# Kernel optimization log

Measured on AMD Instinct MI355X. Metric: run time of the kernel, lower is better.

Reference implementation:

```python
import jax, jax.numpy as jnp
import numpy as np

D_MODEL = 1024
N_HEADS = 16
HEAD_DIM = D_MODEL // N_HEADS
D_FF = 4096
EPS = 1e-5


def _layer_norm(x, gamma, beta):
    mu = jnp.mean(x, axis=-1, keepdims=True)
    var = jnp.var(x, axis=-1, keepdims=True)
    return (x - mu) * jax.lax.rsqrt(var + EPS) * gamma + beta


def setup_inputs() -> dict:
    key = jax.random.key(0)
    ks = jax.random.split(key, 16)
    B, T, S = 2, 2048, 2048
    s = 1.0 / np.sqrt(D_MODEL)
    inp = {
        "tgt": jax.random.normal(ks[0], (B, T, D_MODEL), jnp.float32),
        "memory": jax.random.normal(ks[1], (B, S, D_MODEL), jnp.float32),
        "wq": jax.random.normal(ks[2], (D_MODEL, D_MODEL), jnp.float32) * s,
        "bq": jnp.zeros((D_MODEL,), jnp.float32),
        "wk": jax.random.normal(ks[3], (D_MODEL, D_MODEL), jnp.float32) * s,
        "bk": jnp.zeros((D_MODEL,), jnp.float32),
        "wv": jax.random.normal(ks[4], (D_MODEL, D_MODEL), jnp.float32) * s,
        "bv": jnp.zeros((D_MODEL,), jnp.float32),
        "wo": jax.random.normal(ks[5], (D_MODEL, D_MODEL), jnp.float32) * s,
        "bo": jnp.zeros((D_MODEL,), jnp.float32),
        "w1": jax.random.normal(ks[6], (D_MODEL, D_FF), jnp.float32) * s,
        "b1": jnp.zeros((D_FF,), jnp.float32),
        "w2": jax.random.normal(ks[7], (D_FF, D_MODEL), jnp.float32) * (1.0 / np.sqrt(D_FF)),
        "b2": jnp.zeros((D_MODEL,), jnp.float32),
        "g1": jnp.ones((D_MODEL,), jnp.float32),
        "be1": jnp.zeros((D_MODEL,), jnp.float32),
        "g2": jnp.ones((D_MODEL,), jnp.float32),
        "be2": jnp.zeros((D_MODEL,), jnp.float32),
    }
    return inp


def reference(tgt, memory, wq, bq, wk, bk, wv, bv, wo, bo, w1, b1, w2, b2, g1, be1, g2, be2):
    B, T, _ = tgt.shape
    S = memory.shape[1]
    scale = HEAD_DIM ** -0.5
    # projections -> [B, H, L, Dh]
    Q = (tgt @ wq + bq).reshape(B, T, N_HEADS, HEAD_DIM).transpose(0, 2, 1, 3)
    K = (memory @ wk + bk).reshape(B, S, N_HEADS, HEAD_DIM).transpose(0, 2, 1, 3)
    V = (memory @ wv + bv).reshape(B, S, N_HEADS, HEAD_DIM).transpose(0, 2, 1, 3)
    scores = jnp.einsum("bhtd,bhsd->bhts", Q, K) * scale
    attn = jax.nn.softmax(scores, axis=-1)  # dropout=0 (eval)
    ctx = jnp.einsum("bhts,bhsd->bhtd", attn, V)
    ctx = ctx.transpose(0, 2, 1, 3).reshape(B, T, D_MODEL)
    attn_out = ctx @ wo + bo
    # post-norm residual blocks
    x = _layer_norm(tgt + attn_out, g1, be1)
    ff = jax.nn.relu(x @ w1 + b1) @ w2 + b2
    out = _layer_norm(x + ff, g2, be2)
    return out
```

## Files before the change

kernel.cpp:

```cpp
#include <hip/hip_runtime.h>


typedef unsigned short u16;
typedef __attribute__((ext_vector_type(8))) short bvec8;
typedef __attribute__((ext_vector_type(4))) float fvec4;

#define MFMA16(a, b, c) __builtin_amdgcn_mfma_f32_16x16x32_bf16((a), (b), (c), 0, 0, 0)

__device__ __forceinline__ u16 f2b(float f) {
  union { float f; unsigned u; } x; x.f = f;
  unsigned u = x.u;
  return (u16)((u + 0x7FFFu + ((u >> 16) & 1u)) >> 16);
}
__device__ __forceinline__ u16 f2b_t(float f) {
  union { float f; unsigned u; } x; x.f = f;
  return (u16)(x.u >> 16);
}
__device__ __forceinline__ void gl_lds16(const u16* g, u16* lds) {
  __builtin_amdgcn_global_load_lds(
      (const __attribute__((address_space(1))) void*)g,
      (__attribute__((address_space(3))) void*)lds, 16, 0, 0);
}

__global__ __launch_bounds__(256) void k_tobf(const float* __restrict__ in,
                                              u16* __restrict__ out, int n4) {
  int i = blockIdx.x * 256 + threadIdx.x;
  if (i >= n4) return;
  float4 v = ((const float4*)in)[i];
  ushort4 o;
  o.x = f2b(v.x); o.y = f2b(v.y); o.z = f2b(v.z); o.w = f2b(v.w);
  ((ushort4*)out)[i] = o;
}

__global__ __launch_bounds__(256) void k_wt(const float* __restrict__ W,
                                            u16* __restrict__ WT, int K, int N) {
  __shared__ float t[32][33];
  int tx = threadIdx.x & 31, ty = threadIdx.x >> 5;
  int n0 = blockIdx.x * 32, k0 = blockIdx.y * 32;
#pragma unroll
  for (int i = 0; i < 4; i++)
    t[ty + i * 8][tx] = W[(size_t)(k0 + ty + i * 8) * N + n0 + tx];
  __syncthreads();
#pragma unroll
  for (int i = 0; i < 4; i++)
    WT[(size_t)(n0 + ty + i * 8) * K + k0 + tx] = f2b(t[tx][ty + i * 8]);
}

__global__ __launch_bounds__(256) void k_vt(const u16* __restrict__ V,
                                            u16* __restrict__ Vt) {
  __shared__ u16 t[32][33];
  int tx = threadIdx.x & 31, ty = threadIdx.x >> 5;
  int s0 = blockIdx.x * 32, d0 = blockIdx.y * 32, bh = blockIdx.z;
  int b = bh >> 4, h = bh & 15;
#pragma unroll
  for (int i = 0; i < 4; i++)
    t[ty + i * 8][tx] = V[(size_t)(b * 2048 + s0 + ty + i * 8) * 1024 + h * 64 + d0 + tx];
  __syncthreads();
#pragma unroll
  for (int i = 0; i < 4; i++)
    Vt[((size_t)bh * 64 + d0 + ty + i * 8) * 2048 + s0 + tx] = t[tx][ty + i * 8];
}

template <int TM, int TN>
__global__ __launch_bounds__(256, 3) void k_gemm(
    const u16* __restrict__ A, const u16* __restrict__ BT,
    const float* __restrict__ bias, const float* __restrict__ bias2,
    const float* __restrict__ resid, float* __restrict__ outF,
    u16* __restrict__ outB, u16* __restrict__ outB2,
    int M, int N, int K, float scale, int flags) {
  constexpr int WM = TM / 2, WN = TN / 2;
  constexpr int MI = WM / 16, NI = WN / 16;
  constexpr int NCALL = (TM + TN) / 64;
  __shared__ u16 S[(TM + TN) * 32];
  const int tid = threadIdx.x, w = tid >> 6, lane = tid & 63;
  const int q = lane >> 4, l = lane & 15;
  const int m0 = blockIdx.y * TM, n0 = blockIdx.x * TN;
  const int wm = (w >> 1) * WM, wn = (w & 1) * WN;
  const int srow = lane >> 2, sgrp = lane & 3;
  const int gcol = ((sgrp + (srow >> 1)) & 3) * 8;
  const int rpos = ((q + 4 - ((l >> 1) & 3)) & 3) * 8;
  const u16* gp[NCALL];
  u16* lp[NCALL];
#pragma unroll
  for (int c = 0; c < NCALL; c++) {
    int r0 = (w * NCALL + c) * 16;
    gp[c] = (r0 < TM) ? A + (size_t)(m0 + r0 + srow) * K + gcol
                      : BT + (size_t)(n0 + r0 - TM + srow) * K + gcol;
    lp[c] = &S[r0 * 32];
  }
  fvec4 acc[MI][NI] = {};
#pragma unroll 1
  for (int k0 = 0; k0 < K; k0 += 32) {
#pragma unroll
    for (int c = 0; c < NCALL; c++) gl_lds16(gp[c] + k0, lp[c]);
    __syncthreads();
    bvec8 af[MI], bf[NI];
#pragma unroll
    for (int i = 0; i < MI; i++)
      af[i] = *(const bvec8*)&S[(wm + 16 * i + l) * 32 + rpos];
#pragma unroll
    for (int j = 0; j < NI; j++)
      bf[j] = *(const bvec8*)&S[(TM + wn + 16 * j + l) * 32 + rpos];
#pragma unroll
    for (int i = 0; i < MI; i++)
#pragma unroll
      for (int j = 0; j < NI; j++)
        acc[i][j] = MFMA16(af[i], bf[j], acc[i][j]);
    __syncthreads();
  }
  const int On = outB2 ? 1024 : N;
#pragma unroll
  for (int mi = 0; mi < MI; mi++)
#pragma unroll
    for (int ni = 0; ni < NI; ni++) {
      int row = m0 + wm + mi * 16 + q * 4;
      int col = n0 + wn + ni * 16 + l;
      const float* bs = bias;
      u16* ob = outB;
      float sc = scale;
      int oc = col;
      if (outB2 && col >= 1024) { bs = bias2; ob = outB2; sc = 1.0f; oc = col - 1024; }
      float bv = bs[oc];
#pragma unroll
      for (int r = 0; r < 4; r++) {
        float v = (acc[mi][ni][r] + bv) * sc;
        if (flags & 1) v = fmaxf(v, 0.0f);
        size_t idx = (size_t)(row + r) * On + oc;
        if (flags & 8) v += resid[idx];
        if (flags & 2) ob[idx] = f2b(v);
        if (flags & 4) outF[idx] = v;
      }
    }
}

__global__ __launch_bounds__(256, 2) void k_attn(
    const u16* __restrict__ Q, const u16* __restrict__ Kb,
    const u16* __restrict__ Vt, u16* __restrict__ ctx) {
  __shared__ u16 Ks[64 * 64];
  __shared__ u16 Vs[64 * 64];
  __shared__ u16 Ps[4][2][16 * 72];
  const int tid = threadIdx.x, w = tid >> 6, lane = tid & 63;
  const int q = lane >> 4, l = lane & 15;
  const int blk = blockIdx.x;
  const int bh = blk >> 4, tb = blk & 15;
  const int b = bh >> 4, h = bh & 15;
  const int t0 = tb * 128 + w * 32;
  const u16* Qp = Q + (size_t)(b * 2048 + t0) * 1024 + h * 64;
  const u16* Kp = Kb + (size_t)(b * 2048) * 1024 + h * 64;
  const u16* Vp = Vt + (size_t)bh * 64 * 2048;
  const int rowin = lane >> 3, grp = lane & 7;
  const int gcol = ((grp + rowin) & 7) * 8;
  const int kc0 = ((q + 8 - (l & 7)) & 7) * 8;
  const int kc1 = ((q + 12 - (l & 7)) & 7) * 8;
  bvec8 aQ[2][2];
#pragma unroll
  for (int ti = 0; ti < 2; ti++)
#pragma unroll
    for (int kh = 0; kh < 2; kh++)
      aQ[ti][kh] = *(const bvec8*)&Qp[(size_t)(ti * 16 + l) * 1024 + kh * 32 + q * 8];
  fvec4 o[2][4] = {};
  float ls[2][4] = {};
#pragma unroll 1
  for (int s0 = 0; s0 < 2048; s0 += 64) {
    gl_lds16(Kp + (size_t)(s0 + w * 8 + rowin) * 1024 + gcol, &Ks[(w * 8) * 64]);
    gl_lds16(Kp + (size_t)(s0 + 32 + w * 8 + rowin) * 1024 + gcol, &Ks[(32 + w * 8) * 64]);
    gl_lds16(Vp + (size_t)(w * 8 + rowin) * 2048 + s0 + gcol, &Vs[(w * 8) * 64]);
    gl_lds16(Vp + (size_t)(32 + w * 8 + rowin) * 2048 + s0 + gcol, &Vs[(32 + w * 8) * 64]);
    __syncthreads();
    fvec4 sc[2][4];
#pragma unroll
    for (int ti = 0; ti < 2; ti++)
#pragma unroll
      for (int ss = 0; ss < 4; ss++) sc[ti][ss] = (fvec4){0.f, 0.f, 0.f, 0.f};
#pragma unroll
    for (int ss = 0; ss < 4; ss++) {
      const int ro = (ss * 16 + l) * 64;
      bvec8 kf0 = *(const bvec8*)&Ks[ro + kc0];
      bvec8 kf1 = *(const bvec8*)&Ks[ro + kc1];
#pragma unroll
      for (int ti = 0; ti < 2; ti++) {
        sc[ti][ss] = MFMA16(aQ[ti][0], kf0, sc[ti][ss]);
        sc[ti][ss] = MFMA16(aQ[ti][1], kf1, sc[ti][ss]);
      }
    }
#pragma unroll
    for (int ti = 0; ti < 2; ti++)
#pragma unroll
      for (int ss = 0; ss < 4; ss++)
#pragma unroll
        for (int r = 0; r < 4; r++) {
          float p = __expf(sc[ti][ss][r]);
          ls[ti][r] += p;
          Ps[w][ti][(q * 4 + r) * 72 + ss * 16 + l] = f2b_t(p);
        }
    asm volatile("s_waitcnt lgkmcnt(0)" ::: "memory");
    bvec8 bV[4][2];
#pragma unroll
    for (int dt = 0; dt < 4; dt++) {
      const int ro = (dt * 16 + l) * 64;
      bV[dt][0] = *(const bvec8*)&Vs[ro + kc0];
      bV[dt][1] = *(const bvec8*)&Vs[ro + kc1];
    }
#pragma unroll
    for (int ti = 0; ti < 2; ti++) {
      bvec8 aP0 = *(const bvec8*)&Ps[w][ti][l * 72 + q * 8];
      bvec8 aP1 = *(const bvec8*)&Ps[w][ti][l * 72 + 32 + q * 8];
#pragma unroll
      for (int dt = 0; dt < 4; dt++) {
        o[ti][dt] = MFMA16(aP0, bV[dt][0], o[ti][dt]);
        o[ti][dt] = MFMA16(aP1, bV[dt][1], o[ti][dt]);
      }
    }
    __syncthreads();
  }
#pragma unroll
  for (int ti = 0; ti < 2; ti++)
#pragma unroll
    for (int r = 0; r < 4; r++) {
      float s = ls[ti][r];
      s += __shfl_xor(s, 1, 64);
      s += __shfl_xor(s, 2, 64);
      s += __shfl_xor(s, 4, 64);
      s += __shfl_xor(s, 8, 64);
      float inv = 1.0f / s;
      size_t trow = (size_t)(b * 2048 + t0 + ti * 16 + q * 4 + r);
#pragma unroll
      for (int dt = 0; dt < 4; dt++)
        ctx[trow * 1024 + h * 64 + dt * 16 + l] = f2b(o[ti][dt][r] * inv);
    }
}

__global__ __launch_bounds__(256) void k_ln(
    const float* __restrict__ y, const float* __restrict__ g,
    const float* __restrict__ be, float* __restrict__ xf, u16* __restrict__ xb) {
  __shared__ float sm[8];
  int row = blockIdx.x, tid = threadIdx.x;
  const float* yr = y + (size_t)row * 1024;
  float v[4], s = 0.f, ss = 0.f;
#pragma unroll
  for (int j = 0; j < 4; j++) {
    v[j] = yr[tid + j * 256];
    s += v[j]; ss += v[j] * v[j];
  }
#pragma unroll
  for (int off = 32; off; off >>= 1) {
    s += __shfl_down(s, off, 64);
    ss += __shfl_down(ss, off, 64);
  }
  int w = tid >> 6;
  if ((tid & 63) == 0) { sm[w] = s; sm[4 + w] = ss; }
  __syncthreads();
  float S = sm[0] + sm[1] + sm[2] + sm[3];
  float SS = sm[4] + sm[5] + sm[6] + sm[7];
  float mean = S * (1.0f / 1024.0f);
  float var = SS * (1.0f / 1024.0f) - mean * mean;
  float rstd = rsqrtf(var + 1e-5f);
#pragma unroll
  for (int j = 0; j < 4; j++) {
    int c = tid + j * 256;
    float o = (v[j] - mean) * rstd * g[c] + be[c];
    xf[(size_t)row * 1024 + c] = o;
    if (xb) xb[(size_t)row * 1024 + c] = f2b(o);
  }
}

extern "C" void kernel_launch(void* const* d_in, const int* in_sizes, int n_in,
                              void* d_out, int out_size, void* d_ws, size_t ws_size,
                              hipStream_t stream) {
  (void)in_sizes; (void)n_in; (void)out_size; (void)ws_size;
  const float* tgt = (const float*)d_in[0];
  const float* mem = (const float*)d_in[1];
  const float* wq  = (const float*)d_in[2];
  const float* bq  = (const float*)d_in[3];
  const float* wk  = (const float*)d_in[4];
  const float* bk  = (const float*)d_in[5];
  const float* wv  = (const float*)d_in[6];
  const float* bv  = (const float*)d_in[7];
  const float* wo  = (const float*)d_in[8];
  const float* bo  = (const float*)d_in[9];
  const float* w1  = (const float*)d_in[10];
  const float* b1  = (const float*)d_in[11];
  const float* w2  = (const float*)d_in[12];
  const float* b2  = (const float*)d_in[13];
  const float* g1  = (const float*)d_in[14];
  const float* be1 = (const float*)d_in[15];
  const float* g2  = (const float*)d_in[16];
  const float* be2 = (const float*)d_in[17];
  float* out = (float*)d_out;

  char* ws = (char*)d_ws;
  size_t off = 0;
  auto take = [&](size_t bytes) { char* p = ws + off; off += bytes; return p; };
  const size_t MB = 1024 * 1024;
  u16* tgt_b = (u16*)take(8 * MB);
  u16* mem_b = (u16*)take(8 * MB);
  u16* wqT   = (u16*)take(2 * MB);
  u16* wkvT  = (u16*)take(4 * MB);
  u16* woT   = (u16*)take(2 * MB);
  u16* w1T   = (u16*)take(8 * MB);
  u16* w2T   = (u16*)take(8 * MB);
  u16* Qb    = (u16*)take(8 * MB);
  u16* Kb    = (u16*)take(8 * MB);
  u16* Vb    = (u16*)take(8 * MB);
  u16* Vtb   = (u16*)take(8 * MB);
  u16* ctx   = (u16*)take(8 * MB);
  float* y1  = (float*)take(16 * MB);
  float* xf  = (float*)take(16 * MB);
  u16* xb    = (u16*)take(8 * MB);
  u16* hbuf  = Qb;
  float* y2  = (float*)ctx;

  k_tobf<<<4096, 256, 0, stream>>>(tgt, tgt_b, 4096 * 1024 / 4);
  k_tobf<<<4096, 256, 0, stream>>>(mem, mem_b, 4096 * 1024 / 4);
  k_wt<<<dim3(32, 32), 256, 0, stream>>>(wq, wqT, 1024, 1024);
  k_wt<<<dim3(32, 32), 256, 0, stream>>>(wk, wkvT, 1024, 1024);
  k_wt<<<dim3(32, 32), 256, 0, stream>>>(wv, wkvT + 1024 * 1024, 1024, 1024);
  k_wt<<<dim3(32, 32), 256, 0, stream>>>(wo, woT, 1024, 1024);
  k_wt<<<dim3(128, 32), 256, 0, stream>>>(w1, w1T, 1024, 4096);
  k_wt<<<dim3(32, 128), 256, 0, stream>>>(w2, w2T, 4096, 1024);
  k_gemm<64, 128><<<dim3(8, 64), 256, 0, stream>>>(
      tgt_b, wqT, bq, nullptr, nullptr, nullptr, Qb, nullptr,
      4096, 1024, 1024, 0.125f, 2);
  k_gemm<128, 128><<<dim3(16, 32), 256, 0, stream>>>(
      mem_b, wkvT, bk, bv, nullptr, nullptr, Kb, Vb,
      4096, 2048, 1024, 1.0f, 2);
  k_vt<<<dim3(64, 2, 32), 256, 0, stream>>>(Vb, Vtb);
  k_attn<<<512, 256, 0, stream>>>(Qb, Kb, Vtb, ctx);
  k_gemm<64, 128><<<dim3(8, 64), 256, 0, stream>>>(
      ctx, woT, bo, nullptr, tgt, y1, nullptr, nullptr,
      4096, 1024, 1024, 1.0f, 4 | 8);
  k_ln<<<4096, 256, 0, stream>>>(y1, g1, be1, xf, xb);
  k_gemm<128, 128><<<dim3(32, 32), 256, 0, stream>>>(
      xb, w1T, b1, nullptr, nullptr, nullptr, hbuf, nullptr,
      4096, 4096, 1024, 1.0f, 1 | 2);
  k_gemm<64, 128><<<dim3(8, 64), 256, 0, stream>>>(
      hbuf, w2T, b2, nullptr, xf, y2, nullptr, nullptr,
      4096, 1024, 4096, 1.0f, 4 | 8);
  k_ln<<<4096, 256, 0, stream>>>(y2, g2, be2, out, nullptr);
}
```

Measured before the change: 437.6 us.

## Split-K the N=1024 GEMMs and split-KV the attention to fill more CUs

Attention now runs over two halves of the key sequence in separate blocks. Each half writes unnormalized fp32 partial outputs and row sums, and a new combine kernel adds them and normalizes to bf16. The output-projection and FFN-down GEMMs use a two-way split-K that writes fp32 partials, and a fused kernel adds the partials, bias and residual before the layernorm. Occupancy hints are also raised for the 64-row GEMM and for attention. The aim is to double the grid of launches that were under-filling the GPU, at the cost of extra fp32 partial-buffer traffic and one more launch. Skipping the softmax max is safe only if the scores stay bounded, as the original code already assumed.

```diff
diff --git a/kernel.cpp b/kernel.cpp
--- a/kernel.cpp
+++ b/kernel.cpp
@@ -62,12 +62,12 @@
 }
 
 template <int TM, int TN>
-__global__ __launch_bounds__(256, 3) void k_gemm(
+__global__ __launch_bounds__(256, TM == 64 ? 4 : 3) void k_gemm(
     const u16* __restrict__ A, const u16* __restrict__ BT,
     const float* __restrict__ bias, const float* __restrict__ bias2,
     const float* __restrict__ resid, float* __restrict__ outF,
     u16* __restrict__ outB, u16* __restrict__ outB2,
-    int M, int N, int K, float scale, int flags) {
+    int M, int N, int Kstride, int Klen, float scale, int flags) {
   constexpr int WM = TM / 2, WN = TN / 2;
   constexpr int MI = WM / 16, NI = WN / 16;
   constexpr int NCALL = (TM + TN) / 64;
@@ -75,6 +75,7 @@
   const int tid = threadIdx.x, w = tid >> 6, lane = tid & 63;
   const int q = lane >> 4, l = lane & 15;
   const int m0 = blockIdx.y * TM, n0 = blockIdx.x * TN;
+  const int kbeg = blockIdx.z * Klen;
   const int wm = (w >> 1) * WM, wn = (w & 1) * WN;
   const int srow = lane >> 2, sgrp = lane & 3;
   const int gcol = ((sgrp + (srow >> 1)) & 3) * 8;
@@ -84,13 +85,13 @@
 #pragma unroll
   for (int c = 0; c < NCALL; c++) {
     int r0 = (w * NCALL + c) * 16;
-    gp[c] = (r0 < TM) ? A + (size_t)(m0 + r0 + srow) * K + gcol
-                      : BT + (size_t)(n0 + r0 - TM + srow) * K + gcol;
+    gp[c] = (r0 < TM) ? A + (size_t)(m0 + r0 + srow) * Kstride + kbeg + gcol
+                      : BT + (size_t)(n0 + r0 - TM + srow) * Kstride + kbeg + gcol;
     lp[c] = &S[r0 * 32];
   }
   fvec4 acc[MI][NI] = {};
 #pragma unroll 1
-  for (int k0 = 0; k0 < K; k0 += 32) {
+  for (int k0 = 0; k0 < Klen; k0 += 32) {
 #pragma unroll
     for (int c = 0; c < NCALL; c++) gl_lds16(gp[c] + k0, lp[c]);
     __syncthreads();
@@ -107,6 +108,20 @@
       for (int j = 0; j < NI; j++)
         acc[i][j] = MFMA16(af[i], bf[j], acc[i][j]);
     __syncthreads();
+  }
+  if (flags & 16) {
+    float* po = outF + (size_t)blockIdx.z * M * N;
+#pragma unroll
+    for (int mi = 0; mi < MI; mi++)
+#pragma unroll
+      for (int ni = 0; ni < NI; ni++) {
+        int row = m0 + wm + mi * 16 + q * 4;
+        int col = n0 + wn + ni * 16 + l;
+#pragma unroll
+        for (int r = 0; r < 4; r++)
+          po[(size_t)(row + r) * N + col] = acc[mi][ni][r];
+      }
+    return;
   }
   const int On = outB2 ? 1024 : N;
 #pragma unroll
@@ -133,9 +148,10 @@
     }
 }
 
-__global__ __launch_bounds__(256, 2) void k_attn(
+__global__ __launch_bounds__(256, 4) void k_attn(
     const u16* __restrict__ Q, const u16* __restrict__ Kb,
-    const u16* __restrict__ Vt, u16* __restrict__ ctx) {
+    const u16* __restrict__ Vt, float* __restrict__ opart,
+    float* __restrict__ lpart) {
   __shared__ u16 Ks[64 * 64];
   __shared__ u16 Vs[64 * 64];
   __shared__ u16 Ps[4][2][16 * 72];
@@ -145,6 +161,9 @@
   const int bh = blk >> 4, tb = blk & 15;
   const int b = bh >> 4, h = bh & 15;
   const int t0 = tb * 128 + w * 32;
+  const int sbeg = blockIdx.y * 1024;
+  float* op = opart + (size_t)blockIdx.y * 4096 * 1024;
+  float* lp = lpart + (size_t)blockIdx.y * 4096 * 16;
   const u16* Qp = Q + (size_t)(b * 2048 + t0) * 1024 + h * 64;
   const u16* Kp = Kb + (size_t)(b * 2048) * 1024 + h * 64;
   const u16* Vp = Vt + (size_t)bh * 64 * 2048;
@@ -161,7 +180,7 @@
   fvec4 o[2][4] = {};
   float ls[2][4] = {};
 #pragma unroll 1
-  for (int s0 = 0; s0 < 2048; s0 += 64) {
+  for (int s0 = sbeg; s0 < sbeg + 1024; s0 += 64) {
     gl_lds16(Kp + (size_t)(s0 + w * 8 + rowin) * 1024 + gcol, &Ks[(w * 8) * 64]);
     gl_lds16(Kp + (size_t)(s0 + 32 + w * 8 + rowin) * 1024 + gcol, &Ks[(32 + w * 8) * 64]);
     gl_lds16(Vp + (size_t)(w * 8 + rowin) * 2048 + s0 + gcol, &Vs[(w * 8) * 64]);
@@ -222,24 +241,44 @@
       s += __shfl_xor(s, 2, 64);
       s += __shfl_xor(s, 4, 64);
       s += __shfl_xor(s, 8, 64);
-      float inv = 1.0f / s;
-      size_t trow = (size_t)(b * 2048 + t0 + ti * 16 + q * 4 + r);
+      int trow = b * 2048 + t0 + ti * 16 + q * 4 + r;
+      if (l == 0) lp[trow * 16 + h] = s;
 #pragma unroll
       for (int dt = 0; dt < 4; dt++)
-        ctx[trow * 1024 + h * 64 + dt * 16 + l] = f2b(o[ti][dt][r] * inv);
-    }
-}
-
-__global__ __launch_bounds__(256) void k_ln(
-    const float* __restrict__ y, const float* __restrict__ g,
-    const float* __restrict__ be, float* __restrict__ xf, u16* __restrict__ xb) {
+        op[(size_t)trow * 1024 + h * 64 + dt * 16 + l] = o[ti][dt][r];
+    }
+}
+
+__global__ __launch_bounds__(256) void k_actx(const float* __restrict__ opart,
+                                              const float* __restrict__ lpart,
+                                              u16* __restrict__ ctx) {
+  int row = blockIdx.x, c0 = threadIdx.x * 4;
+  int h = c0 >> 6;
+  float lsum = lpart[row * 16 + h] + lpart[4096 * 16 + row * 16 + h];
+  float inv = 1.0f / lsum;
+  float4 a = *(const float4*)&opart[(size_t)row * 1024 + c0];
+  float4 b = *(const float4*)&opart[(size_t)4096 * 1024 + (size_t)row * 1024 + c0];
+  ushort4 o;
+  o.x = f2b((a.x + b.x) * inv);
+  o.y = f2b((a.y + b.y) * inv);
+  o.z = f2b((a.z + b.z) * inv);
+  o.w = f2b((a.w + b.w) * inv);
+  *(ushort4*)&ctx[(size_t)row * 1024 + c0] = o;
+}
+
+__global__ __launch_bounds__(256) void k_lnp(
+    const float* __restrict__ p0, const float* __restrict__ p1,
+    const float* __restrict__ bias, const float* __restrict__ resid,
+    const float* __restrict__ g, const float* __restrict__ be,
+    float* __restrict__ xf, u16* __restrict__ xb) {
   __shared__ float sm[8];
   int row = blockIdx.x, tid = threadIdx.x;
-  const float* yr = y + (size_t)row * 1024;
+  size_t base = (size_t)row * 1024;
   float v[4], s = 0.f, ss = 0.f;
 #pragma unroll
   for (int j = 0; j < 4; j++) {
-    v[j] = yr[tid + j * 256];
+    int c = tid + j * 256;
+    v[j] = p0[base + c] + p1[base + c] + bias[c] + resid[base + c];
     s += v[j]; ss += v[j] * v[j];
   }
 #pragma unroll
@@ -259,8 +298,8 @@
   for (int j = 0; j < 4; j++) {
     int c = tid + j * 256;
     float o = (v[j] - mean) * rstd * g[c] + be[c];
-    xf[(size_t)row * 1024 + c] = o;
-    if (xb) xb[(size_t)row * 1024 + c] = f2b(o);
+    xf[base + c] = o;
+    if (xb) xb[base + c] = f2b(o);
   }
 }
 
@@ -304,11 +343,13 @@
   u16* Vb    = (u16*)take(8 * MB);
   u16* Vtb   = (u16*)take(8 * MB);
   u16* ctx   = (u16*)take(8 * MB);
-  float* y1  = (float*)take(16 * MB);
+  float* opart = (float*)take(32 * MB);
+  float* lpart = (float*)take(1 * MB);
+  float* opj   = (float*)take(32 * MB);
   float* xf  = (float*)take(16 * MB);
   u16* xb    = (u16*)take(8 * MB);
   u16* hbuf  = Qb;
-  float* y2  = (float*)ctx;
+  float* fp2 = opart;
 
   k_tobf<<<4096, 256, 0, stream>>>(tgt, tgt_b, 4096 * 1024 / 4);
   k_tobf<<<4096, 256, 0, stream>>>(mem, mem_b, 4096 * 1024 / 4);
@@ -320,21 +361,22 @@
   k_wt<<<dim3(32, 128), 256, 0, stream>>>(w2, w2T, 4096, 1024);
   k_gemm<64, 128><<<dim3(8, 64), 256, 0, stream>>>(
       tgt_b, wqT, bq, nullptr, nullptr, nullptr, Qb, nullptr,
-      4096, 1024, 1024, 0.125f, 2);
+      4096, 1024, 1024, 1024, 0.125f, 2);
   k_gemm<128, 128><<<dim3(16, 32), 256, 0, stream>>>(
       mem_b, wkvT, bk, bv, nullptr, nullptr, Kb, Vb,
-      4096, 2048, 1024, 1.0f, 2);
+      4096, 2048, 1024, 1024, 1.0f, 2);
   k_vt<<<dim3(64, 2, 32), 256, 0, stream>>>(Vb, Vtb);
-  k_attn<<<512, 256, 0, stream>>>(Qb, Kb, Vtb, ctx);
-  k_gemm<64, 128><<<dim3(8, 64), 256, 0, stream>>>(
-      ctx, woT, bo, nullptr, tgt, y1, nullptr, nullptr,
-      4096, 1024, 1024, 1.0f, 4 | 8);
-  k_ln<<<4096, 256, 0, stream>>>(y1, g1, be1, xf, xb);
+  k_attn<<<dim3(512, 2), 256, 0, stream>>>(Qb, Kb, Vtb, opart, lpart);
+  k_actx<<<4096, 256, 0, stream>>>(opart, lpart, ctx);
+  k_gemm<64, 128><<<dim3(8, 64, 2), 256, 0, stream>>>(
+      ctx, woT, nullptr, nullptr, nullptr, opj, nullptr, nullptr,
+      4096, 1024, 1024, 512, 1.0f, 16);
+  k_lnp<<<4096, 256, 0, stream>>>(opj, opj + 4096 * 1024, bo, tgt, g1, be1, xf, xb);
   k_gemm<128, 128><<<dim3(32, 32), 256, 0, stream>>>(
       xb, w1T, b1, nullptr, nullptr, nullptr, hbuf, nullptr,
-      4096, 4096, 1024, 1.0f, 1 | 2);
-  k_gemm<64, 128><<<dim3(8, 64), 256, 0, stream>>>(
-      hbuf, w2T, b2, nullptr, xf, y2, nullptr, nullptr,
-      4096, 1024, 4096, 1.0f, 4 | 8);
-  k_ln<<<4096, 256, 0, stream>>>(y2, g2, be2, out, nullptr);
-}
+      4096, 4096, 1024, 1024, 1.0f, 1 | 2);
+  k_gemm<64, 128><<<dim3(8, 64, 2), 256, 0, stream>>>(
+      hbuf, w2T, nullptr, nullptr, nullptr, fp2, nullptr, nullptr,
+      4096, 1024, 4096, 2048, 1.0f, 16);
+  k_lnp<<<4096, 256, 0, stream>>>(fp2, fp2 + 4096 * 1024, b2, xf, g2, be2, out, nullptr);
+}
```

Measured after the change: 424.5 us. 3.0% less time.
